# Optimization experiments

Hardware: AMD Instinct MI355X
Metric: run time of the kernel (lower is better)

## Reference

```python
import jax, jax.numpy as jnp
import numpy as np

N = 10000
E = 160000
IN_DIM = 128
OUT_DIM = 32
HEADS = 32
H1 = OUT_DIM * 2   # 64 per-head channels in layer 1
H2 = OUT_DIM       # 32 per-head channels in layer 2
NEG_SLOPE = 0.2
EPS = 1e-16  # PyG softmax denominator epsilon


def gat_layer(x, src, dst, W, a_src, a_dst, b, n_nodes, heads, ch):
    # x: [N, F_in], W: [F_in, heads*ch], a_src/a_dst: [heads, ch], b: [ch]
    xp = (x @ W).reshape(n_nodes, heads, ch)                 # [N,H,C]
    alpha_s = jnp.einsum('nhc,hc->nh', xp, a_src)            # [N,H]
    alpha_d = jnp.einsum('nhc,hc->nh', xp, a_dst)            # [N,H]
    e = jax.nn.leaky_relu(alpha_s[src] + alpha_d[dst], NEG_SLOPE)  # [E,H]
    # segment softmax over edges grouped by destination node
    m = jax.ops.segment_max(e, dst, num_segments=n_nodes)    # [N,H]
    e = jnp.exp(e - m[dst])                                  # [E,H]
    s = jax.ops.segment_sum(e, dst, num_segments=n_nodes)    # [N,H]
    alpha = e / (s[dst] + EPS)                               # [E,H]
    msg = alpha[:, :, None] * xp[src]                        # [E,H,C]
    out = jax.ops.segment_sum(msg, dst, num_segments=n_nodes)  # [N,H,C]
    return out.mean(axis=1) + b                              # concat=False: head mean, [N,C]


def setup_inputs() -> dict:
    key = jax.random.key(0)
    ks = jax.random.split(key, 9)
    x = jax.random.normal(ks[0], (N, IN_DIM), dtype=jnp.float32)
    edge_index = jax.random.randint(ks[1], (2, E), 0, N, dtype=jnp.int64)
    W1 = jax.random.normal(ks[2], (IN_DIM, HEADS * H1), dtype=jnp.float32) * 0.1
    a_src1 = jax.random.normal(ks[3], (HEADS, H1), dtype=jnp.float32) * 0.1
    a_dst1 = jax.random.normal(ks[4], (HEADS, H1), dtype=jnp.float32) * 0.1
    b1 = jnp.zeros((H1,), dtype=jnp.float32)
    W2 = jax.random.normal(ks[5], (H1, HEADS * H2), dtype=jnp.float32) * 0.1
    a_src2 = jax.random.normal(ks[6], (HEADS, H2), dtype=jnp.float32) * 0.1
    a_dst2 = jax.random.normal(ks[7], (HEADS, H2), dtype=jnp.float32) * 0.1
    b2 = jnp.zeros((H2,), dtype=jnp.float32)
    return {"x": x, "edge_index": edge_index,
            "W1": W1, "a_src1": a_src1, "a_dst1": a_dst1, "b1": b1,
            "W2": W2, "a_src2": a_src2, "a_dst2": a_dst2, "b2": b2}


def reference(x, edge_index, W1, a_src1, a_dst1, b1, W2, a_src2, a_dst2, b2):
    # flow='source_to_target': messages go edge_index[0] -> edge_index[1]
    src = edge_index[0]
    dst = edge_index[1]
    z1 = jax.nn.elu(gat_layer(x, src, dst, W1, a_src1, a_dst1, b1, N, HEADS, H1))
    z2 = jax.nn.elu(gat_layer(z1, src, dst, W2, a_src2, a_dst2, b2, N, HEADS, H2))
    return jnp.concatenate((z1, z2), axis=-1)  # [N, 96]
```

## Files before the change

### kernel.cpp

```cpp
#include <hip/hip_runtime.h>
#include <hip/hip_bf16.h>

#define NN 10000
#define NE 160000
#define NH 32
#define LRELU_SLOPE 0.2f
#define SM_EPS 1e-16f
#define SM_SHIFT 16.0f

typedef __hip_bfloat16 bf16;
typedef __attribute__((ext_vector_type(8))) __bf16 bf16x8;
typedef __attribute__((ext_vector_type(4))) float f32x4;

__device__ __forceinline__ float asf(unsigned int u) {
    union { unsigned int u; float f; } v; v.u = u; return v.f;
}

__global__ void k_detect_zero(const unsigned int* __restrict__ raw, int* __restrict__ flag,
                              int* __restrict__ deg) {
    int i = blockIdx.x * blockDim.x + threadIdx.x;
    if (i < NN) deg[i] = 0;
    if (i == 0) {
        int z = 1;
        for (int j = 1; j < 32; j += 2) z &= (raw[j] == 0u);
        *flag = z;
    }
}
__global__ void k_norm_hist(const int* __restrict__ raw, const int* __restrict__ flag,
                            int* __restrict__ srcv, int* __restrict__ dstv, int* __restrict__ deg) {
    int e = blockIdx.x * blockDim.x + threadIdx.x;
    if (e >= NE) return;
    int s, d;
    if (*flag) { s = raw[2 * e]; d = raw[2 * (NE + e)]; }
    else       { s = raw[e];     d = raw[NE + e]; }
    srcv[e] = s; dstv[e] = d;
    atomicAdd(&deg[d], 1);
}
__global__ void k_scan(const int* __restrict__ deg, int* __restrict__ offs, int* __restrict__ cursor) {
    __shared__ int wsum[16], wpre[16];
    __shared__ int base;
    const int tid = threadIdx.x, lane = tid & 63, wid = tid >> 6;
    if (tid == 0) base = 0;
    __syncthreads();
    for (int chunk = 0; chunk < NN; chunk += 1024) {
        int idx = chunk + tid;
        int v = (idx < NN) ? deg[idx] : 0;
        int s = v;
        #pragma unroll
        for (int off = 1; off < 64; off <<= 1) {
            int t = __shfl_up(s, off);
            if (lane >= off) s += t;
        }
        if (lane == 63) wsum[wid] = s;
        __syncthreads();
        if (wid == 0) {
            int ws = (lane < 16) ? wsum[lane] : 0;
            #pragma unroll
            for (int off = 1; off < 16; off <<= 1) {
                int t = __shfl_up(ws, off);
                if (lane >= off) ws += t;
            }
            if (lane < 16) wpre[lane] = ws;
        }
        __syncthreads();
        int wbase = (wid == 0) ? 0 : wpre[wid - 1];
        int excl = base + wbase + s - v;
        if (idx < NN) { offs[idx] = excl; cursor[idx] = excl; }
        int total = wpre[15];
        __syncthreads();
        if (tid == 0) base += total;
        __syncthreads();
    }
    if (tid == 0) offs[NN] = base;
}
__global__ void k_scatter(const int* __restrict__ srcv, const int* __restrict__ dstv,
                          int* __restrict__ cursor, int* __restrict__ srcs,
                          int* __restrict__ dstp) {
    int e = blockIdx.x * blockDim.x + threadIdx.x;
    if (e < NE) {
        int d = dstv[e];
        int p = atomicAdd(&cursor[d], 1);
        srcs[p] = srcv[e];
        dstp[p] = d;
    }
}

__global__ void k_prep(const float* __restrict__ X, bf16* __restrict__ Xb,
                       const float* __restrict__ W1, bf16* __restrict__ Wt1,
                       const float* __restrict__ W2, bf16* __restrict__ Wt2) {
    int i = blockIdx.x * blockDim.x + threadIdx.x;
    if (i < NN * 128) { Xb[i] = __float2bfloat16(X[i]); return; }
    i -= NN * 128;
    if (i < 128 * 2048) {
        int k = i / 2048, m = i - k * 2048;
        Wt1[(size_t)m * 128 + k] = __float2bfloat16(W1[i]);
        return;
    }
    i -= 128 * 2048;
    if (i < 64 * 1024) {
        int k = i / 1024, m = i - k * 1024;
        Wt2[(size_t)m * 64 + k] = __float2bfloat16(W2[i]);
    }
}

template<int K, int M, int C>
__global__ __launch_bounds__(256) void k_gemm_mfma(
        const bf16* __restrict__ Xb, const bf16* __restrict__ Wt,
        const float* __restrict__ Asrc, const float* __restrict__ Adst,
        bf16* __restrict__ XPB, float* __restrict__ aS, float* __restrict__ aD) {
    constexpr int BM = 64, BN = 128;
    constexpr int KB = K * 2;
    constexpr int NHB = BN / C;
    constexpr int WPH = C / 32;
    __shared__ char lds[(BM + BN) * KB];
    __shared__ float sredS[4][BM], sredD[4][BM];
    char* lA = lds;
    char* lB = lds + BM * KB;

    const int tid = threadIdx.x;
    const int wv = tid >> 6, ln = tid & 63;
    const int lrow = ln & 15, lkb = ln >> 4;
    const int brow = blockIdx.x * BM;
    const int bcol = blockIdx.y * BN;

    #pragma unroll
    for (int c = 0; c < BM * K / 8 / 256; c++) {
        int it = c * 256 + tid;
        int r = it / (K / 8), kc = (it % (K / 8)) * 8;
        int node = brow + r;
        uint4 v = make_uint4(0u, 0u, 0u, 0u);
        if (node < NN) v = *reinterpret_cast<const uint4*>(&Xb[(size_t)node * K + kc]);
        *reinterpret_cast<uint4*>(lA + ((r * KB + kc * 2) ^ ((r & 7) << 4))) = v;
    }
    #pragma unroll
    for (int c = 0; c < BN * K / 8 / 256; c++) {
        int it = c * 256 + tid;
        int r = it / (K / 8), kc = (it % (K / 8)) * 8;
        uint4 v = *reinterpret_cast<const uint4*>(&Wt[(size_t)(bcol + r) * K + kc]);
        *reinterpret_cast<uint4*>(lB + ((r * KB + kc * 2) ^ ((r & 7) << 4))) = v;
    }
    __syncthreads();

    f32x4 acc[4][2];
    #pragma unroll
    for (int mi = 0; mi < 4; mi++)
        #pragma unroll
        for (int nj = 0; nj < 2; nj++) acc[mi][nj] = (f32x4){0.f, 0.f, 0.f, 0.f};

    #pragma unroll
    for (int ks = 0; ks < K / 32; ks++) {
        const int k0 = ks * 32 + lkb * 8;
        bf16x8 af[4], bfr[2];
        #pragma unroll
        for (int mi = 0; mi < 4; mi++) {
            int r = mi * 16 + lrow;
            af[mi] = *reinterpret_cast<const bf16x8*>(lA + ((r * KB + k0 * 2) ^ ((r & 7) << 4)));
        }
        #pragma unroll
        for (int nj = 0; nj < 2; nj++) {
            int r = wv * 32 + nj * 16 + lrow;
            bfr[nj] = *reinterpret_cast<const bf16x8*>(lB + ((r * KB + k0 * 2) ^ ((r & 7) << 4)));
        }
        #pragma unroll
        for (int mi = 0; mi < 4; mi++)
            #pragma unroll
            for (int nj = 0; nj < 2; nj++)
                acc[mi][nj] = __builtin_amdgcn_mfma_f32_16x16x32_bf16(af[mi], bfr[nj], acc[mi][nj], 0, 0, 0);
    }

    float ar0 = Asrc[bcol + wv * 32 + lrow];
    float ar1 = Asrc[bcol + wv * 32 + 16 + lrow];
    float ad0 = Adst[bcol + wv * 32 + lrow];
    float ad1 = Adst[bcol + wv * 32 + 16 + lrow];

    #pragma unroll
    for (int mi = 0; mi < 4; mi++) {
        #pragma unroll
        for (int r = 0; r < 4; r++) {
            int rowl = mi * 16 + lkb * 4 + r;
            int row = brow + rowl;
            if (row < NN) {
                XPB[(size_t)row * M + bcol + wv * 32 + lrow]      = __float2bfloat16(acc[mi][0][r]);
                XPB[(size_t)row * M + bcol + wv * 32 + 16 + lrow] = __float2bfloat16(acc[mi][1][r]);
            }
            float vs = acc[mi][0][r] * ar0 + acc[mi][1][r] * ar1;
            float vd = acc[mi][0][r] * ad0 + acc[mi][1][r] * ad1;
            vs += __shfl_xor(vs, 1); vd += __shfl_xor(vd, 1);
            vs += __shfl_xor(vs, 2); vd += __shfl_xor(vd, 2);
            vs += __shfl_xor(vs, 4); vd += __shfl_xor(vd, 4);
            vs += __shfl_xor(vs, 8); vd += __shfl_xor(vd, 8);
            if (lrow == 0) {
                sredS[wv][rowl] = vs;
                sredD[wv][rowl] = vd;
            }
        }
    }
    __syncthreads();
    if (tid < BM) {
        int node = brow + tid;
        if (node < NN) {
            #pragma unroll
            for (int hb = 0; hb < NHB; hb++) {
                float ss = 0.f, dd = 0.f;
                #pragma unroll
                for (int w = 0; w < WPH; w++) {
                    ss += sredS[hb * WPH + w][tid];
                    dd += sredD[hb * WPH + w][tid];
                }
                int h = bcol / C + hb;
                aS[node * NH + h] = ss;
                aD[node * NH + h] = dd;
            }
        }
    }
}

__global__ __launch_bounds__(256) void k_score_edge(
        const float* __restrict__ aS, const float* __restrict__ aD,
        const int* __restrict__ srcs, const int* __restrict__ dstp,
        float* __restrict__ pEh) {
    const int i = blockIdx.x * 256 + threadIdx.x;
    const int s = srcs[i];
    const int d = dstp[i];
    const float4* prs = reinterpret_cast<const float4*>(&aS[s * NH]);
    const float4* prd = reinterpret_cast<const float4*>(&aD[d * NH]);
    float4 vs[8], vd[8];
    #pragma unroll
    for (int j = 0; j < 8; j++) { vs[j] = prs[j]; vd[j] = prd[j]; }
    #pragma unroll
    for (int j = 0; j < 8; j++) {
        float sc, p;
        sc = vs[j].x + vd[j].x; sc = (sc >= 0.f) ? sc : LRELU_SLOPE * sc;
        p = __expf(sc - SM_SHIFT); pEh[(size_t)(4 * j + 0) * NE + i] = p;
        sc = vs[j].y + vd[j].y; sc = (sc >= 0.f) ? sc : LRELU_SLOPE * sc;
        p = __expf(sc - SM_SHIFT); pEh[(size_t)(4 * j + 1) * NE + i] = p;
        sc = vs[j].z + vd[j].z; sc = (sc >= 0.f) ? sc : LRELU_SLOPE * sc;
        p = __expf(sc - SM_SHIFT); pEh[(size_t)(4 * j + 2) * NE + i] = p;
        sc = vs[j].w + vd[j].w; sc = (sc >= 0.f) ? sc : LRELU_SLOPE * sc;
        p = __expf(sc - SM_SHIFT); pEh[(size_t)(4 * j + 3) * NE + i] = p;
    }
}

template<int C>
__global__ __launch_bounds__(256) void k_agg_slice(
        const bf16* __restrict__ XPB, const float* __restrict__ pEh,
        const int* __restrict__ offs, const int* __restrict__ srcs,
        float* __restrict__ P, int sg0) {
    constexpr int M = NH * C;
    constexpr int HPS = 128 / C;
    constexpr int CGH = C / 8;
    const int sg = sg0 + (blockIdx.x & 7);
    const int wid = threadIdx.x >> 6, lane = threadIdx.x & 63;
    const int node = (blockIdx.x >> 3) * 4 + wid;
    const int cg = lane & 15, el = lane >> 4;
    const int hl = cg / CGH;
    const int h = sg * HPS + hl;
    const int col = sg * 128 + cg * 8;
    const int beg = offs[node], end = offs[node + 1];
    const float* __restrict__ pErow = pEh + (size_t)h * NE;
    float acc[8];
    #pragma unroll
    for (int j = 0; j < 8; j++) acc[j] = 0.f;
    float ssum = 0.f;
    int i = beg + el;
    int sN = 0; float pN = 0.f;
    if (i < end) { sN = srcs[i]; pN = pErow[i]; }
    while (i < end) {
        const int s = sN; const float p = pN;
        const int i2 = i + 4;
        if (i2 < end) { sN = srcs[i2]; pN = pErow[i2]; }
        uint4 v = *reinterpret_cast<const uint4*>(&XPB[(size_t)s * M + col]);
        ssum += p;
        acc[0] = fmaf(p, asf(v.x << 16),          acc[0]);
        acc[1] = fmaf(p, asf(v.x & 0xffff0000u),  acc[1]);
        acc[2] = fmaf(p, asf(v.y << 16),          acc[2]);
        acc[3] = fmaf(p, asf(v.y & 0xffff0000u),  acc[3]);
        acc[4] = fmaf(p, asf(v.z << 16),          acc[4]);
        acc[5] = fmaf(p, asf(v.z & 0xffff0000u),  acc[5]);
        acc[6] = fmaf(p, asf(v.w << 16),          acc[6]);
        acc[7] = fmaf(p, asf(v.w & 0xffff0000u),  acc[7]);
        i = i2;
    }
    #pragma unroll
    for (int j = 0; j < 8; j++) {
        acc[j] += __shfl_xor(acc[j], 16);
        acc[j] += __shfl_xor(acc[j], 32);
    }
    ssum += __shfl_xor(ssum, 16);
    ssum += __shfl_xor(ssum, 32);
    const float r = 1.f / (ssum + SM_EPS);
    #pragma unroll
    for (int j = 0; j < 8; j++) acc[j] *= r;
    #pragma unroll
    for (int j = 0; j < 8; j++) acc[j] += __shfl_xor(acc[j], 8);
    if constexpr (HPS == 4) {
        #pragma unroll
        for (int j = 0; j < 8; j++) acc[j] += __shfl_xor(acc[j], 4);
    }
    if (el == 0 && cg < CGH) {
        float* dst = &P[((size_t)sg * NN + node) * C + cg * 8];
        *reinterpret_cast<float4*>(dst)     = make_float4(acc[0], acc[1], acc[2], acc[3]);
        *reinterpret_cast<float4*>(dst + 4) = make_float4(acc[4], acc[5], acc[6], acc[7]);
    }
}

template<int C, int NS, bool WZ>
__global__ void k_reduce(const float* __restrict__ P, const float* __restrict__ bias,
                         float* __restrict__ out, int col0, bf16* __restrict__ z1b) {
    constexpr int TPN = C / 4;
    const int tid = threadIdx.x;
    const int node = blockIdx.x * (256 / TPN) + tid / TPN;
    const int c = (tid % TPN) * 4;
    if (node >= NN) return;
    float4 s = make_float4(0.f, 0.f, 0.f, 0.f);
    #pragma unroll
    for (int sg = 0; sg < NS; sg++) {
        float4 v = *reinterpret_cast<const float4*>(&P[((size_t)sg * NN + node) * C + c]);
        s.x += v.x; s.y += v.y; s.z += v.z; s.w += v.w;
    }
    float4 b = *reinterpret_cast<const float4*>(&bias[c]);
    s.x = s.x * (1.0f / NH) + b.x;
    s.y = s.y * (1.0f / NH) + b.y;
    s.z = s.z * (1.0f / NH) + b.z;
    s.w = s.w * (1.0f / NH) + b.w;
    s.x = (s.x > 0.f) ? s.x : expm1f(s.x);
    s.y = (s.y > 0.f) ? s.y : expm1f(s.y);
    s.z = (s.z > 0.f) ? s.z : expm1f(s.z);
    s.w = (s.w > 0.f) ? s.w : expm1f(s.w);
    *reinterpret_cast<float4*>(&out[(size_t)node * 96 + col0 + c]) = s;
    if constexpr (WZ) {
        bf16 hx[4] = {__float2bfloat16(s.x), __float2bfloat16(s.y),
                      __float2bfloat16(s.z), __float2bfloat16(s.w)};
        *reinterpret_cast<uint2*>(&z1b[(size_t)node * C + c]) =
            *reinterpret_cast<const uint2*>(hx);
    }
}

extern "C" void kernel_launch(void* const* d_in, const int* in_sizes, int n_in,
                              void* d_out, int out_size, void* d_ws, size_t ws_size,
                              hipStream_t stream) {
    const float* x   = (const float*)d_in[0];
    const int*   ei  = (const int*)d_in[1];
    const float* W1  = (const float*)d_in[2];
    const float* as1 = (const float*)d_in[3];
    const float* ad1 = (const float*)d_in[4];
    const float* b1  = (const float*)d_in[5];
    const float* W2  = (const float*)d_in[6];
    const float* as2 = (const float*)d_in[7];
    const float* ad2 = (const float*)d_in[8];
    const float* b2  = (const float*)d_in[9];
    float* out = (float*)d_out;

    char* w = (char*)d_ws;
    size_t off = 0;
    auto alloc = [&](size_t bytes) -> void* {
        void* p = w + off;
        off = (off + bytes + 255) & ~(size_t)255;
        return p;
    };
    bf16*  xpb    = (bf16*)alloc((size_t)NN * 2048 * 2);
    float* aS     = (float*)alloc((size_t)NN * NH * 4);
    float* aD     = (float*)alloc((size_t)NN * NH * 4);
    float* pEh    = (float*)alloc((size_t)NH * NE * 4);
    float* P1     = (float*)alloc((size_t)16 * NN * 64 * 4);
    float* P2     = P1;
    int*   deg    = (int*)alloc((size_t)NN * 4);
    int*   cursor = (int*)alloc((size_t)NN * 4);
    int*   offs   = (int*)alloc((size_t)(NN + 1) * 4);
    int*   srcs   = (int*)alloc((size_t)NE * 4);
    int*   dstp   = (int*)alloc((size_t)NE * 4);
    int*   srcv   = (int*)alloc((size_t)NE * 4);
    int*   dstv   = (int*)alloc((size_t)NE * 4);
    bf16*  Xb     = (bf16*)alloc((size_t)NN * 128 * 2);
    bf16*  Wt1    = (bf16*)alloc((size_t)2048 * 128 * 2);
    bf16*  Wt2    = (bf16*)alloc((size_t)1024 * 64 * 2);
    bf16*  z1b    = (bf16*)alloc((size_t)NN * 64 * 2);
    int*   eflag  = (int*)alloc(256);
    (void)ws_size; (void)in_sizes; (void)n_in; (void)out_size;

    k_detect_zero<<<(NN + 255) / 256, 256, 0, stream>>>((const unsigned int*)ei, eflag, deg);
    k_norm_hist<<<NE / 256, 256, 0, stream>>>(ei, eflag, srcv, dstv, deg);
    k_scan<<<1, 1024, 0, stream>>>(deg, offs, cursor);
    k_scatter<<<NE / 256, 256, 0, stream>>>(srcv, dstv, cursor, srcs, dstp);

    k_prep<<<(NN * 128 + 128 * 2048 + 64 * 1024 + 255) / 256, 256, 0, stream>>>(
        x, Xb, W1, Wt1, W2, Wt2);

    k_gemm_mfma<128, 2048, 64><<<dim3((NN + 63) / 64, 2048 / 128), 256, 0, stream>>>(
        Xb, Wt1, as1, ad1, xpb, aS, aD);
    k_score_edge<<<NE / 256, 256, 0, stream>>>(aS, aD, srcs, dstp, pEh);
    k_agg_slice<64><<<(NN / 4) * 8, 256, 0, stream>>>(xpb, pEh, offs, srcs, P1, 0);
    k_agg_slice<64><<<(NN / 4) * 8, 256, 0, stream>>>(xpb, pEh, offs, srcs, P1, 8);
    k_reduce<64, 16, true><<<NN / 16, 256, 0, stream>>>(P1, b1, out, 0, z1b);

    k_gemm_mfma<64, 1024, 32><<<dim3((NN + 63) / 64, 1024 / 128), 256, 0, stream>>>(
        z1b, Wt2, as2, ad2, xpb, aS, aD);
    k_score_edge<<<NE / 256, 256, 0, stream>>>(aS, aD, srcs, dstp, pEh);
    k_agg_slice<32><<<(NN / 4) * 8, 256, 0, stream>>>(xpb, pEh, offs, srcs, P2, 0);
    k_reduce<32, 8, false><<<(NN * 8 + 255) / 256, 256, 0, stream>>>(P2, b2, out, 64, nullptr);
}
```

Baseline: 237.6 us.

## Pad CSR segments to multiples of four and unroll aggregation loop

The degree scan now rounds each destination segment up to a multiple of four. Padding slots get src=0 and dst=-1, and the score kernel writes zero probabilities for them. This lets the aggregation loop use a fixed trip count with two-way unrolling and no per-iteration bounds checks or prefetch logic. The two layer-1 aggregation launches are merged into one double-sized grid, and k_prep moves before scatter to initialise the padding. In exchange the score kernel processes extra padded edges, and the padding adds dummy gathers of node 0.

```diff
diff --git a/kernel.cpp b/kernel.cpp
--- a/kernel.cpp
+++ b/kernel.cpp
@@ -3,6 +3,7 @@
 
 #define NN 10000
 #define NE 160000
+#define NE_PAD 190464
 #define NH 32
 #define LRELU_SLOPE 0.2f
 #define SM_EPS 1e-16f
@@ -44,7 +45,7 @@
     __syncthreads();
     for (int chunk = 0; chunk < NN; chunk += 1024) {
         int idx = chunk + tid;
-        int v = (idx < NN) ? deg[idx] : 0;
+        int v = (idx < NN) ? ((deg[idx] + 3) & ~3) : 0;
         int s = v;
         #pragma unroll
         for (int off = 1; off < 64; off <<= 1) {
@@ -87,8 +88,10 @@
 
 __global__ void k_prep(const float* __restrict__ X, bf16* __restrict__ Xb,
                        const float* __restrict__ W1, bf16* __restrict__ Wt1,
-                       const float* __restrict__ W2, bf16* __restrict__ Wt2) {
+                       const float* __restrict__ W2, bf16* __restrict__ Wt2,
+                       int* __restrict__ srcs, int* __restrict__ dstp) {
     int i = blockIdx.x * blockDim.x + threadIdx.x;
+    if (i < NE_PAD) { srcs[i] = 0; dstp[i] = -1; }
     if (i < NN * 128) { Xb[i] = __float2bfloat16(X[i]); return; }
     i -= NN * 128;
     if (i < 128 * 2048) {
@@ -220,8 +223,13 @@
         const int* __restrict__ srcs, const int* __restrict__ dstp,
         float* __restrict__ pEh) {
     const int i = blockIdx.x * 256 + threadIdx.x;
+    const int d = dstp[i];
+    if (d < 0) {
+        #pragma unroll
+        for (int h = 0; h < NH; h++) pEh[(size_t)h * NE_PAD + i] = 0.f;
+        return;
+    }
     const int s = srcs[i];
-    const int d = dstp[i];
     const float4* prs = reinterpret_cast<const float4*>(&aS[s * NH]);
     const float4* prd = reinterpret_cast<const float4*>(&aD[d * NH]);
     float4 vs[8], vd[8];
@@ -231,13 +239,13 @@
     for (int j = 0; j < 8; j++) {
         float sc, p;
         sc = vs[j].x + vd[j].x; sc = (sc >= 0.f) ? sc : LRELU_SLOPE * sc;
-        p = __expf(sc - SM_SHIFT); pEh[(size_t)(4 * j + 0) * NE + i] = p;
+        p = __expf(sc - SM_SHIFT); pEh[(size_t)(4 * j + 0) * NE_PAD + i] = p;
         sc = vs[j].y + vd[j].y; sc = (sc >= 0.f) ? sc : LRELU_SLOPE * sc;
-        p = __expf(sc - SM_SHIFT); pEh[(size_t)(4 * j + 1) * NE + i] = p;
+        p = __expf(sc - SM_SHIFT); pEh[(size_t)(4 * j + 1) * NE_PAD + i] = p;
         sc = vs[j].z + vd[j].z; sc = (sc >= 0.f) ? sc : LRELU_SLOPE * sc;
-        p = __expf(sc - SM_SHIFT); pEh[(size_t)(4 * j + 2) * NE + i] = p;
+        p = __expf(sc - SM_SHIFT); pEh[(size_t)(4 * j + 2) * NE_PAD + i] = p;
         sc = vs[j].w + vd[j].w; sc = (sc >= 0.f) ? sc : LRELU_SLOPE * sc;
-        p = __expf(sc - SM_SHIFT); pEh[(size_t)(4 * j + 3) * NE + i] = p;
+        p = __expf(sc - SM_SHIFT); pEh[(size_t)(4 * j + 3) * NE_PAD + i] = p;
     }
 }
 
@@ -245,42 +253,48 @@
 __global__ __launch_bounds__(256) void k_agg_slice(
         const bf16* __restrict__ XPB, const float* __restrict__ pEh,
         const int* __restrict__ offs, const int* __restrict__ srcs,
-        float* __restrict__ P, int sg0) {
+        float* __restrict__ P) {
     constexpr int M = NH * C;
     constexpr int HPS = 128 / C;
     constexpr int CGH = C / 8;
-    const int sg = sg0 + (blockIdx.x & 7);
+    constexpr int HGRID = (NN / 4) * 8;
+    int b = blockIdx.x;
+    const int hp = (b >= HGRID) ? 1 : 0;
+    b -= hp * HGRID;
+    const int sg = (b & 7) + hp * 8;
     const int wid = threadIdx.x >> 6, lane = threadIdx.x & 63;
-    const int node = (blockIdx.x >> 3) * 4 + wid;
+    const int node = (b >> 3) * 4 + wid;
     const int cg = lane & 15, el = lane >> 4;
     const int hl = cg / CGH;
     const int h = sg * HPS + hl;
     const int col = sg * 128 + cg * 8;
     const int beg = offs[node], end = offs[node + 1];
-    const float* __restrict__ pErow = pEh + (size_t)h * NE;
+    const float* __restrict__ pErow = pEh + (size_t)h * NE_PAD;
     float acc[8];
     #pragma unroll
     for (int j = 0; j < 8; j++) acc[j] = 0.f;
     float ssum = 0.f;
     int i = beg + el;
-    int sN = 0; float pN = 0.f;
-    if (i < end) { sN = srcs[i]; pN = pErow[i]; }
-    while (i < end) {
-        const int s = sN; const float p = pN;
-        const int i2 = i + 4;
-        if (i2 < end) { sN = srcs[i2]; pN = pErow[i2]; }
-        uint4 v = *reinterpret_cast<const uint4*>(&XPB[(size_t)s * M + col]);
-        ssum += p;
-        acc[0] = fmaf(p, asf(v.x << 16),          acc[0]);
-        acc[1] = fmaf(p, asf(v.x & 0xffff0000u),  acc[1]);
-        acc[2] = fmaf(p, asf(v.y << 16),          acc[2]);
-        acc[3] = fmaf(p, asf(v.y & 0xffff0000u),  acc[3]);
-        acc[4] = fmaf(p, asf(v.z << 16),          acc[4]);
-        acc[5] = fmaf(p, asf(v.z & 0xffff0000u),  acc[5]);
-        acc[6] = fmaf(p, asf(v.w << 16),          acc[6]);
-        acc[7] = fmaf(p, asf(v.w & 0xffff0000u),  acc[7]);
-        i = i2;
-    }
+    const int trip = (end - beg) >> 2;
+    #define AGG_STEP(ii) { \
+        const int s_ = srcs[ii]; const float p_ = pErow[ii]; \
+        uint4 v_ = *reinterpret_cast<const uint4*>(&XPB[(size_t)s_ * M + col]); \
+        ssum += p_; \
+        acc[0] = fmaf(p_, asf(v_.x << 16),         acc[0]); \
+        acc[1] = fmaf(p_, asf(v_.x & 0xffff0000u), acc[1]); \
+        acc[2] = fmaf(p_, asf(v_.y << 16),         acc[2]); \
+        acc[3] = fmaf(p_, asf(v_.y & 0xffff0000u), acc[3]); \
+        acc[4] = fmaf(p_, asf(v_.z << 16),         acc[4]); \
+        acc[5] = fmaf(p_, asf(v_.z & 0xffff0000u), acc[5]); \
+        acc[6] = fmaf(p_, asf(v_.w << 16),         acc[6]); \
+        acc[7] = fmaf(p_, asf(v_.w & 0xffff0000u), acc[7]); }
+    if (trip & 1) { AGG_STEP(i); i += 4; }
+    for (int t = trip >> 1; t > 0; t--) {
+        AGG_STEP(i);
+        AGG_STEP(i + 4);
+        i += 8;
+    }
+    #undef AGG_STEP
     #pragma unroll
     for (int j = 0; j < 8; j++) {
         acc[j] += __shfl_xor(acc[j], 16);
@@ -361,14 +375,14 @@
     bf16*  xpb    = (bf16*)alloc((size_t)NN * 2048 * 2);
     float* aS     = (float*)alloc((size_t)NN * NH * 4);
     float* aD     = (float*)alloc((size_t)NN * NH * 4);
-    float* pEh    = (float*)alloc((size_t)NH * NE * 4);
+    float* pEh    = (float*)alloc((size_t)NH * NE_PAD * 4);
     float* P1     = (float*)alloc((size_t)16 * NN * 64 * 4);
     float* P2     = P1;
     int*   deg    = (int*)alloc((size_t)NN * 4);
     int*   cursor = (int*)alloc((size_t)NN * 4);
     int*   offs   = (int*)alloc((size_t)(NN + 1) * 4);
-    int*   srcs   = (int*)alloc((size_t)NE * 4);
-    int*   dstp   = (int*)alloc((size_t)NE * 4);
+    int*   srcs   = (int*)alloc((size_t)NE_PAD * 4);
+    int*   dstp   = (int*)alloc((size_t)NE_PAD * 4);
     int*   srcv   = (int*)alloc((size_t)NE * 4);
     int*   dstv   = (int*)alloc((size_t)NE * 4);
     bf16*  Xb     = (bf16*)alloc((size_t)NN * 128 * 2);
@@ -381,21 +395,19 @@
     k_detect_zero<<<(NN + 255) / 256, 256, 0, stream>>>((const unsigned int*)ei, eflag, deg);
     k_norm_hist<<<NE / 256, 256, 0, stream>>>(ei, eflag, srcv, dstv, deg);
     k_scan<<<1, 1024, 0, stream>>>(deg, offs, cursor);
+    k_prep<<<(NN * 128 + 128 * 2048 + 64 * 1024 + 255) / 256, 256, 0, stream>>>(
+        x, Xb, W1, Wt1, W2, Wt2, srcs, dstp);
     k_scatter<<<NE / 256, 256, 0, stream>>>(srcv, dstv, cursor, srcs, dstp);
-
-    k_prep<<<(NN * 128 + 128 * 2048 + 64 * 1024 + 255) / 256, 256, 0, stream>>>(
-        x, Xb, W1, Wt1, W2, Wt2);
 
     k_gemm_mfma<128, 2048, 64><<<dim3((NN + 63) / 64, 2048 / 128), 256, 0, stream>>>(
         Xb, Wt1, as1, ad1, xpb, aS, aD);
-    k_score_edge<<<NE / 256, 256, 0, stream>>>(aS, aD, srcs, dstp, pEh);
-    k_agg_slice<64><<<(NN / 4) * 8, 256, 0, stream>>>(xpb, pEh, offs, srcs, P1, 0);
-    k_agg_slice<64><<<(NN / 4) * 8, 256, 0, stream>>>(xpb, pEh, offs, srcs, P1, 8);
+    k_score_edge<<<NE_PAD / 256, 256, 0, stream>>>(aS, aD, srcs, dstp, pEh);
+    k_agg_slice<64><<<(NN / 4) * 16, 256, 0, stream>>>(xpb, pEh, offs, srcs, P1);
     k_reduce<64, 16, true><<<NN / 16, 256, 0, stream>>>(P1, b1, out, 0, z1b);
 
     k_gemm_mfma<64, 1024, 32><<<dim3((NN + 63) / 64, 1024 / 128), 256, 0, stream>>>(
         z1b, Wt2, as2, ad2, xpb, aS, aD);
-    k_score_edge<<<NE / 256, 256, 0, stream>>>(aS, aD, srcs, dstp, pEh);
-    k_agg_slice<32><<<(NN / 4) * 8, 256, 0, stream>>>(xpb, pEh, offs, srcs, P2, 0);
+    k_score_edge<<<NE_PAD / 256, 256, 0, stream>>>(aS, aD, srcs, dstp, pEh);
+    k_agg_slice<32><<<(NN / 4) * 8, 256, 0, stream>>>(xpb, pEh, offs, srcs, P2);
     k_reduce<32, 8, false><<<(NN * 8 + 255) / 256, 256, 0, stream>>>(P2, b2, out, 64, nullptr);
 }
```

Result: no change. 233.2 us (-1.8%).
